# Kernel optimization log

Measured on AMD Instinct MI355X. Metric: run time of the kernel, lower is better.

Reference implementation:

```python
import jax, jax.numpy as jnp
import numpy as np

B, S, D = 4, 2048, 1024
H, E = 8, 128  # num_head, num_dim (per-head)

def setup_inputs() -> dict:
    key = jax.random.key(0)
    ks = jax.random.split(key, 8)
    scale_in = 1.0 / np.sqrt(D)
    return {
        "q": jax.random.normal(ks[0], (B, S, D), dtype=jnp.float32),
        "k": jax.random.normal(ks[1], (B, S, D), dtype=jnp.float32),
        "v": jax.random.normal(ks[2], (B, S, D), dtype=jnp.float32),
        "Wq": jax.random.normal(ks[3], (H, D, E), dtype=jnp.float32) * scale_in,
        "Wk": jax.random.normal(ks[4], (H, D, E), dtype=jnp.float32) * scale_in,
        "Wv": jax.random.normal(ks[5], (H, D, E), dtype=jnp.float32) * scale_in,
        "Wo": jax.random.normal(ks[6], (H * E, D), dtype=jnp.float32) * (1.0 / np.sqrt(H * E)),
        "bo": jnp.zeros((D,), dtype=jnp.float32),
    }

def reference(q, k, v, Wq, Wk, Wv, Wo, bo):
    dk = jnp.asarray(E, q.dtype) ** 0.5
    # per-head projections, all heads batched: [B,H,S,E]
    qh = jnp.einsum("bsd,hde->bhse", q, Wq)
    kh = jnp.einsum("bsd,hde->bhse", k, Wk)
    vh = jnp.einsum("bsd,hde->bhse", v, Wv)
    scores = jnp.einsum("bhse,bhte->bhst", qh / dk, kh)  # [B,H,S,S]
    attn = jax.nn.softmax(scores, axis=-1)
    zh = jnp.einsum("bhst,bhte->bhse", attn, vh)  # [B,H,S,E]
    # concat heads along feature dim (head order preserved): [B,S,H*E]
    z = jnp.transpose(zh, (0, 2, 1, 3)).reshape(B, S, H * E)
    return z @ Wo + bo
```

## Files before the change

### kernel.cpp

```cpp
#include <hip/hip_runtime.h>

#define B_ 4
#define S_ 2048
#define D_ 1024
#define H_ 8
#define E_ 128

typedef __bf16 bf16_t;
typedef __bf16 bf16x8 __attribute__((ext_vector_type(8)));
typedef float f32x4 __attribute__((ext_vector_type(4)));

#define MFMA16(a, b, c) __builtin_amdgcn_mfma_f32_16x16x32_bf16(a, b, c, 0, 0, 0)

#define LDP_ 72

__device__ __forceinline__ void load_lds16(const bf16_t* g, bf16_t* l) {
    __builtin_amdgcn_global_load_lds(
        (const __attribute__((address_space(1))) unsigned int*)g,
        (__attribute__((address_space(3))) unsigned int*)l,
        16, 0, 0);
}

__device__ __forceinline__ f32x4 zero4() {
    f32x4 z = {0.f, 0.f, 0.f, 0.f};
    return z;
}

__global__ __launch_bounds__(64) void detect_dtype(const unsigned int* __restrict__ q,
                                                   int* __restrict__ flag) {
    int lane = threadIdx.x;
    int cnt = 0;
    for (int i = lane; i < 4096; i += 64) {
        unsigned e = (q[i] >> 7) & 0xFFu;
        cnt += (e >= 110u && e <= 141u) ? 1 : 0;
    }
#pragma unroll
    for (int d = 32; d; d >>= 1) cnt += __shfl_down(cnt, d);
    if (lane == 0) *flag = (cnt > 2048) ? 1 : 0;
}

__global__ __launch_bounds__(256) void convert_bf16(const void* __restrict__ p0,
                                                    const void* __restrict__ p1,
                                                    const void* __restrict__ p2,
                                                    bf16_t* __restrict__ out,
                                                    const int* __restrict__ flagp) {
    const size_t QSZ = (size_t)B_ * H_ * S_ * E_;
    int z = blockIdx.z;
    const void* in = (z == 0) ? p0 : (z == 1) ? p1 : p2;
    bf16_t* o = out + (size_t)z * QSZ;
    int isb = *flagp;
    size_t i = ((size_t)blockIdx.x * 256 + threadIdx.x) * 8;
    if (isb) {
        *(bf16x8*)(o + i) = *(const bf16x8*)((const bf16_t*)in + i);
    } else {
        const float* p = (const float*)in + i;
        f32x4 lo = *(const f32x4*)p;
        f32x4 hi = *(const f32x4*)(p + 4);
        bf16x8 v;
#pragma unroll
        for (int j = 0; j < 4; j++) { v[j] = (bf16_t)lo[j]; v[4 + j] = (bf16_t)hi[j]; }
        *(bf16x8*)(o + i) = v;
    }
}

__global__ __launch_bounds__(256) void transpose_any(const void* __restrict__ p0,
                                                     const void* __restrict__ p1,
                                                     const void* __restrict__ p2,
                                                     bf16_t* __restrict__ out,
                                                     int R, int C,
                                                     const int* __restrict__ flagp) {
    __shared__ bf16_t tile[32][33];
    int isb = *flagp;
    int bz = blockIdx.z;
    int sel = bz >> 3, sub = bz & 7;
    const void* in = (sel == 0) ? p0 : (sel == 1) ? p1 : p2;
    const bf16_t* inb16 = (const bf16_t*)in + (size_t)sub * R * C;
    const float*  inb32 = (const float*)in + (size_t)sub * R * C;
    bf16_t* outb = out + (size_t)bz * R * C;
    int tx = threadIdx.x & 31, ty = threadIdx.x >> 5;
    int r0 = blockIdx.y * 32, c0 = blockIdx.x * 32;
#pragma unroll
    for (int i = 0; i < 4; i++) {
        size_t idx = (size_t)(r0 + ty + i * 8) * C + c0 + tx;
        tile[ty + i * 8][tx] = isb ? inb16[idx] : (bf16_t)inb32[idx];
    }
    __syncthreads();
#pragma unroll
    for (int i = 0; i < 4; i++)
        outb[(size_t)(c0 + ty + i * 8) * R + r0 + tx] = tile[tx][ty + i * 8];
}

__global__ __launch_bounds__(256) void proj_gemm(const bf16_t* __restrict__ Abase,
                                                 int useZ,
                                                 const bf16_t* __restrict__ WtBase,
                                                 bf16_t* __restrict__ OutBase,
                                                 float qscale, int z0) {
    __shared__ __align__(16) bf16_t Alds[128 * 64];
    __shared__ __align__(16) bf16_t Blds[128 * 64];
    const size_t WSZ = (size_t)H_ * E_ * D_;
    const size_t QSZ = (size_t)B_ * H_ * S_ * E_;
    int z = z0 + blockIdx.z;
    const bf16_t* A = Abase + (useZ ? (size_t)z * QSZ : 0);
    const bf16_t* Bt = WtBase + (size_t)z * WSZ + (size_t)blockIdx.y * E_ * D_;
    bf16_t* Out = OutBase + (size_t)z * QSZ;
    int vmode = (z == 2);
    float oscale = (z == 0) ? qscale : 1.0f;

    int m0 = blockIdx.x * 128;
    int h = blockIdx.y;
    int t = threadIdx.x;
    int w = t >> 6, lane = t & 63;
    int quad = lane >> 4, ln = lane & 15;
    int wm = (w >> 1) * 64, wn = (w & 1) * 64;

    f32x4 acc[4][4];
#pragma unroll
    for (int i = 0; i < 4; i++)
#pragma unroll
        for (int j = 0; j < 4; j++) acc[i][j] = zero4();

    for (int k0 = 0; k0 < D_; k0 += 64) {
#pragma unroll
        for (int j = 0; j < 4; j++) {
            int base = j * 256 + w * 64;
            int G = base + lane;
            int r = G >> 3, sl = G & 7;
            int c = sl ^ (r & 7);
            load_lds16(A + (size_t)(m0 + r) * D_ + k0 + c * 8, Alds + (size_t)base * 8);
            load_lds16(Bt + (size_t)r * D_ + k0 + c * 8, Blds + (size_t)base * 8);
        }
        asm volatile("s_waitcnt vmcnt(0)" ::: "memory");
        __syncthreads();

        const bf16_t* Xsrc = vmode ? Blds : Alds;
        const bf16_t* Ysrc = vmode ? Alds : Blds;
#pragma unroll
        for (int ks = 0; ks < 2; ks++) {
            bf16x8 xf[4], yf[4];
#pragma unroll
            for (int mt = 0; mt < 4; mt++) {
                int row = wm + mt * 16 + ln;
                xf[mt] = *(const bf16x8*)(Xsrc + (size_t)row * 64 +
                                          (((ks << 2) + quad) ^ (row & 7)) * 8);
            }
#pragma unroll
            for (int nt = 0; nt < 4; nt++) {
                int row = wn + nt * 16 + ln;
                yf[nt] = *(const bf16x8*)(Ysrc + (size_t)row * 64 +
                                          (((ks << 2) + quad) ^ (row & 7)) * 8);
            }
#pragma unroll
            for (int mt = 0; mt < 4; mt++)
#pragma unroll
                for (int nt = 0; nt < 4; nt++)
                    acc[mt][nt] = MFMA16(xf[mt], yf[nt], acc[mt][nt]);
        }
        __syncthreads();
    }

#pragma unroll
    for (int mt = 0; mt < 4; mt++) {
#pragma unroll
        for (int nt = 0; nt < 4; nt++) {
#pragma unroll
            for (int r = 0; r < 4; r++) {
                int M = wm + mt * 16 + quad * 4 + r;
                int N = wn + nt * 16 + ln;
                float v = acc[mt][nt][r] * oscale;
                size_t idx;
                if (vmode == 0) {
                    int g = m0 + M;
                    int b = g >> 11, s = g & 2047;
                    idx = ((size_t)((b * H_ + h) * S_ + s)) * E_ + N;
                } else {
                    int g = m0 + N;
                    int b = g >> 11, s = g & 2047;
                    idx = ((size_t)((b * H_ + h) * E_ + M)) * S_ + s;
                }
                Out[idx] = (bf16_t)v;
            }
        }
    }
}

__global__ __launch_bounds__(256, 2) void flash_attn(const bf16_t* __restrict__ Qh,
                                                     const bf16_t* __restrict__ Kh,
                                                     const bf16_t* __restrict__ Vt,
                                                     bf16_t* __restrict__ Z) {
    __shared__ __align__(16) bf16_t Klds[64 * 128];
    __shared__ __align__(16) bf16_t Vlds[128 * 64];
    __shared__ __align__(16) bf16_t Plds[4 * 32 * LDP_];
    int bh = blockIdx.y;
    int qt = blockIdx.x;
    const bf16_t* Qbh = Qh + (size_t)bh * S_ * E_;
    const bf16_t* Kbh = Kh + (size_t)bh * S_ * E_;
    const bf16_t* Vbh = Vt + (size_t)bh * E_ * S_;
    int t = threadIdx.x, w = t >> 6, lane = t & 63;
    int quad = lane >> 4, ln = lane & 15;
    bf16_t* Pw = Plds + w * 32 * LDP_;

    bf16x8 qf[2][4];
#pragma unroll
    for (int mt = 0; mt < 2; mt++)
#pragma unroll
        for (int ks = 0; ks < 4; ks++)
            qf[mt][ks] = *(const bf16x8*)(Qbh + (size_t)(qt * 128 + w * 32 + mt * 16 + ln) * E_ +
                                          ks * 32 + quad * 8);

    f32x4 oacc[2][8];
#pragma unroll
    for (int mt = 0; mt < 2; mt++)
#pragma unroll
        for (int nt = 0; nt < 8; nt++) oacc[mt][nt] = zero4();
    float rsum[2][4];
#pragma unroll
    for (int mt = 0; mt < 2; mt++)
#pragma unroll
        for (int r = 0; r < 4; r++) rsum[mt][r] = 0.f;

    int koff[4], voff[4], ldso[4];
#pragma unroll
    for (int j = 0; j < 4; j++) {
        int base = j * 256 + w * 64;
        int G = base + lane;
        int rK = G >> 4, cK = (G & 15) ^ (rK & 15);
        int rV = G >> 3, cV = (G & 7) ^ (rV & 7);
        koff[j] = rK * E_ + cK * 8;
        voff[j] = rV * S_ + cV * 8;
        ldso[j] = G * 8;
    }

    bf16x8 gK[4], gV[4];
#pragma unroll
    for (int j = 0; j < 4; j++) {
        gK[j] = *(const bf16x8*)(Kbh + koff[j]);
        gV[j] = *(const bf16x8*)(Vbh + voff[j]);
    }

    const int NT = S_ / 64;
    for (int kt = 0; kt < NT; kt++) {
#pragma unroll
        for (int j = 0; j < 4; j++) {
            *(bf16x8*)(Klds + ldso[j]) = gK[j];
            *(bf16x8*)(Vlds + ldso[j]) = gV[j];
        }
        __syncthreads();

        int ktn = (kt + 1 < NT) ? kt + 1 : kt;
#pragma unroll
        for (int j = 0; j < 4; j++) {
            gK[j] = *(const bf16x8*)(Kbh + (size_t)ktn * 64 * E_ + koff[j]);
            gV[j] = *(const bf16x8*)(Vbh + ktn * 64 + voff[j]);
        }
        __builtin_amdgcn_sched_barrier(0);

#pragma unroll
        for (int half = 0; half < 2; half++) {
#pragma unroll
            for (int ntl = 0; ntl < 2; ntl++) {
                int nt = half * 2 + ntl;
                f32x4 sacc[2];
                sacc[0] = zero4();
                sacc[1] = zero4();
                __builtin_amdgcn_s_setprio(1);
#pragma unroll
                for (int ks = 0; ks < 4; ks++) {
                    int n = nt * 16 + ln;
                    bf16x8 kf = *(const bf16x8*)(Klds + (size_t)n * 128 +
                                                 (((ks * 4 + quad) ^ ln) & 15) * 8);
#pragma unroll
                    for (int mt = 0; mt < 2; mt++) sacc[mt] = MFMA16(qf[mt][ks], kf, sacc[mt]);
                }
                __builtin_amdgcn_s_setprio(0);
#pragma unroll
                for (int mt = 0; mt < 2; mt++) {
#pragma unroll
                    for (int r = 0; r < 4; r++) {
                        float p = exp2f(sacc[mt][r] - 18.0f);
                        rsum[mt][r] += p;
                        Pw[(size_t)(mt * 16 + quad * 4 + r) * LDP_ + nt * 16 + ln] = (bf16_t)p;
                    }
                }
            }

            asm volatile("s_waitcnt lgkmcnt(0)" ::: "memory");
            {
                int ks = half;
                bf16x8 pf[2], vf[8];
#pragma unroll
                for (int mt = 0; mt < 2; mt++)
                    pf[mt] = *(const bf16x8*)(Pw + (size_t)(mt * 16 + ln) * LDP_ +
                                              ks * 32 + quad * 8);
#pragma unroll
                for (int nt = 0; nt < 8; nt++) {
                    int n = nt * 16 + ln;
                    vf[nt] = *(const bf16x8*)(Vlds + (size_t)n * 64 +
                                              (((ks * 4 + quad) ^ n) & 7) * 8);
                }
                __builtin_amdgcn_s_setprio(1);
#pragma unroll
                for (int mt = 0; mt < 2; mt++)
#pragma unroll
                    for (int nt = 0; nt < 8; nt++)
                        oacc[mt][nt] = MFMA16(pf[mt], vf[nt], oacc[mt][nt]);
                __builtin_amdgcn_s_setprio(0);
            }
        }
        __syncthreads();
    }

    float lr[2][4];
#pragma unroll
    for (int mt = 0; mt < 2; mt++)
#pragma unroll
        for (int r = 0; r < 4; r++) {
            float v = rsum[mt][r];
#pragma unroll
            for (int d = 1; d < 16; d <<= 1) v += __shfl_xor(v, d);
            lr[mt][r] = v;
        }

    int b = bh >> 3, h = bh & 7;
#pragma unroll
    for (int mt = 0; mt < 2; mt++) {
#pragma unroll
        for (int nt = 0; nt < 8; nt++) {
#pragma unroll
            for (int r = 0; r < 4; r++) {
                int s = qt * 128 + w * 32 + mt * 16 + quad * 4 + r;
                int col = h * E_ + nt * 16 + ln;
                Z[((size_t)(b * S_ + s)) * (H_ * E_) + col] =
                    (bf16_t)(oacc[mt][nt][r] / lr[mt][r]);
            }
        }
    }
}

__global__ __launch_bounds__(256) void final_gemm(const bf16_t* __restrict__ A,
                                                  const bf16_t* __restrict__ Bt,
                                                  const void* __restrict__ bias,
                                                  void* __restrict__ Out,
                                                  const int* __restrict__ flagp) {
    __shared__ __align__(16) bf16_t Alds[128 * 64];
    __shared__ __align__(16) bf16_t Blds[128 * 64];
    int isb = *flagp;
    int m0 = blockIdx.x * 128;
    int n0 = blockIdx.y * 128;
    int t = threadIdx.x;
    int w = t >> 6, lane = t & 63;
    int quad = lane >> 4, ln = lane & 15;
    int wm = (w >> 1) * 64, wn = (w & 1) * 64;

    f32x4 acc[4][4];
#pragma unroll
    for (int i = 0; i < 4; i++)
#pragma unroll
        for (int j = 0; j < 4; j++) acc[i][j] = zero4();

    for (int k0 = 0; k0 < D_; k0 += 64) {
#pragma unroll
        for (int j = 0; j < 4; j++) {
            int base = j * 256 + w * 64;
            int G = base + lane;
            int r = G >> 3, sl = G & 7;
            int c = sl ^ (r & 7);
            load_lds16(A + (size_t)(m0 + r) * (H_ * E_) + k0 + c * 8, Alds + (size_t)base * 8);
            load_lds16(Bt + (size_t)(n0 + r) * (H_ * E_) + k0 + c * 8, Blds + (size_t)base * 8);
        }
        asm volatile("s_waitcnt vmcnt(0)" ::: "memory");
        __syncthreads();

#pragma unroll
        for (int ks = 0; ks < 2; ks++) {
            bf16x8 af[4], bfr[4];
#pragma unroll
            for (int mt = 0; mt < 4; mt++) {
                int row = wm + mt * 16 + ln;
                af[mt] = *(const bf16x8*)(Alds + (size_t)row * 64 +
                                          (((ks << 2) + quad) ^ (row & 7)) * 8);
            }
#pragma unroll
            for (int nt = 0; nt < 4; nt++) {
                int row = wn + nt * 16 + ln;
                bfr[nt] = *(const bf16x8*)(Blds + (size_t)row * 64 +
                                           (((ks << 2) + quad) ^ (row & 7)) * 8);
            }
#pragma unroll
            for (int mt = 0; mt < 4; mt++)
#pragma unroll
                for (int nt = 0; nt < 4; nt++)
                    acc[mt][nt] = MFMA16(af[mt], bfr[nt], acc[mt][nt]);
        }
        __syncthreads();
    }

#pragma unroll
    for (int mt = 0; mt < 4; mt++) {
#pragma unroll
        for (int nt = 0; nt < 4; nt++) {
#pragma unroll
            for (int r = 0; r < 4; r++) {
                int grow = m0 + wm + mt * 16 + quad * 4 + r;
                int col = n0 + wn + nt * 16 + ln;
                float bv = isb ? (float)((const bf16_t*)bias)[col]
                               : ((const float*)bias)[col];
                float v = acc[mt][nt][r] + bv;
                size_t idx = (size_t)grow * D_ + col;
                if (isb) ((bf16_t*)Out)[idx] = (bf16_t)v;
                else     ((float*)Out)[idx] = v;
            }
        }
    }
}

extern "C" void kernel_launch(void* const* d_in, const int* in_sizes, int n_in,
                              void* d_out, int out_size, void* d_ws, size_t ws_size,
                              hipStream_t stream) {
    const void* q  = d_in[0];
    const void* k  = d_in[1];
    const void* v  = d_in[2];
    const void* Wq = d_in[3];
    const void* Wk = d_in[4];
    const void* Wv = d_in[5];
    const void* Wo = d_in[6];
    const void* bo = d_in[7];

    int* flag = (int*)d_ws;
    bf16_t* arena = (bf16_t*)((char*)d_ws + 256);
    const size_t WSZ = (size_t)H_ * E_ * D_;
    const size_t QSZ = (size_t)B_ * H_ * S_ * E_;
    bf16_t* wqt = arena;
    bf16_t* wot = wqt + 3 * WSZ;

    const size_t bigBytes = 256 + 2 * (4 * WSZ + 6 * QSZ);
    const bool big = (ws_size >= bigBytes);

    dim3 blk(256);
    const float qscale = 0.08838834764831845f * 1.44269504088896340f;

    detect_dtype<<<dim3(1), dim3(64), 0, stream>>>((const unsigned int*)q, flag);
    transpose_any<<<dim3(4, 32, 24), blk, 0, stream>>>(Wq, Wk, Wv, wqt, D_, E_, flag);
    transpose_any<<<dim3(32, 32, 1), blk, 0, stream>>>(Wo, Wo, Wo, wot, H_ * E_, D_, flag);

    if (big) {
        bf16_t* conv0 = wot + WSZ;
        bf16_t* Qh = conv0 + 3 * QSZ;
        bf16_t* Kh = Qh + QSZ;
        bf16_t* Vt = Kh + QSZ;
        bf16_t* Z  = conv0;

        convert_bf16<<<dim3(4096, 1, 3), blk, 0, stream>>>(q, k, v, conv0, flag);
        proj_gemm<<<dim3(64, 8, 3), blk, 0, stream>>>(conv0, 1, wqt, Qh, qscale, 0);
        flash_attn<<<dim3(16, 32), blk, 0, stream>>>(Qh, Kh, Vt, Z);
        final_gemm<<<dim3(64, 8), blk, 0, stream>>>(Z, wot, bo, d_out, flag);
    } else {
        bf16_t* conv = wot + WSZ;
        bf16_t* Qh = conv + QSZ;
        bf16_t* Kh = Qh + QSZ;
        bf16_t* Vt = Kh + QSZ;
        bf16_t* Z  = conv;

        convert_bf16<<<dim3(4096, 1, 1), blk, 0, stream>>>(q, q, q, conv, flag);
        proj_gemm<<<dim3(64, 8, 1), blk, 0, stream>>>(conv, 0, wqt, Qh, qscale, 0);
        convert_bf16<<<dim3(4096, 1, 1), blk, 0, stream>>>(k, k, k, conv, flag);
        proj_gemm<<<dim3(64, 8, 1), blk, 0, stream>>>(conv, 0, wqt, Qh, qscale, 1);
        convert_bf16<<<dim3(4096, 1, 1), blk, 0, stream>>>(v, v, v, conv, flag);
        proj_gemm<<<dim3(64, 8, 1), blk, 0, stream>>>(conv, 0, wqt, Qh, qscale, 2);
        flash_attn<<<dim3(16, 32), blk, 0, stream>>>(Qh, Kh, Vt, Z);
        final_gemm<<<dim3(64, 8), blk, 0, stream>>>(Z, wot, bo, d_out, flag);
    }
}
```

Before: 374.5 us.

## Transpose QK^T MFMA operands to write P as packed rows and simplify row-sum

Swaps the MFMA operand order so each lane holds four consecutive key columns of one query row. P can then be stored to LDS as a packed 4-element bf16 vector instead of four scalar stores, and the row sum becomes one accumulator per lane reduced with two shuffles. The PV MFMAs now run once per tile after all four score subtiles, instead of interleaved per half, and the final normalization multiplies by a reciprocal instead of dividing. This cuts LDS store instructions and reduction work, but removes the interleaving of exp work with PV MFMAs.

```diff
diff --git a/kernel.cpp b/kernel.cpp
--- a/kernel.cpp
+++ b/kernel.cpp
@@ -7,6 +7,7 @@
 #define E_ 128
 
 typedef __bf16 bf16_t;
+typedef __bf16 bf16x4 __attribute__((ext_vector_type(4)));
 typedef __bf16 bf16x8 __attribute__((ext_vector_type(8)));
 typedef float f32x4 __attribute__((ext_vector_type(4)));
 
@@ -212,11 +213,7 @@
     for (int mt = 0; mt < 2; mt++)
 #pragma unroll
         for (int nt = 0; nt < 8; nt++) oacc[mt][nt] = zero4();
-    float rsum[2][4];
-#pragma unroll
-    for (int mt = 0; mt < 2; mt++)
-#pragma unroll
-        for (int r = 0; r < 4; r++) rsum[mt][r] = 0.f;
+    float rsum[2] = {0.f, 0.f};
 
     int koff[4], voff[4], ldso[4];
 #pragma unroll
@@ -255,70 +252,67 @@
         __builtin_amdgcn_sched_barrier(0);
 
 #pragma unroll
-        for (int half = 0; half < 2; half++) {
-#pragma unroll
-            for (int ntl = 0; ntl < 2; ntl++) {
-                int nt = half * 2 + ntl;
-                f32x4 sacc[2];
-                sacc[0] = zero4();
-                sacc[1] = zero4();
-                __builtin_amdgcn_s_setprio(1);
-#pragma unroll
-                for (int ks = 0; ks < 4; ks++) {
-                    int n = nt * 16 + ln;
-                    bf16x8 kf = *(const bf16x8*)(Klds + (size_t)n * 128 +
-                                                 (((ks * 4 + quad) ^ ln) & 15) * 8);
-#pragma unroll
-                    for (int mt = 0; mt < 2; mt++) sacc[mt] = MFMA16(qf[mt][ks], kf, sacc[mt]);
+        for (int nt = 0; nt < 4; nt++) {
+            f32x4 sacc[2];
+            sacc[0] = zero4();
+            sacc[1] = zero4();
+            __builtin_amdgcn_s_setprio(1);
+#pragma unroll
+            for (int ks = 0; ks < 4; ks++) {
+                int n = nt * 16 + ln;
+                bf16x8 kf = *(const bf16x8*)(Klds + (size_t)n * 128 +
+                                             (((ks * 4 + quad) ^ ln) & 15) * 8);
+#pragma unroll
+                for (int mt = 0; mt < 2; mt++) sacc[mt] = MFMA16(kf, qf[mt][ks], sacc[mt]);
+            }
+            __builtin_amdgcn_s_setprio(0);
+#pragma unroll
+            for (int mt = 0; mt < 2; mt++) {
+                bf16x4 pk;
+#pragma unroll
+                for (int r = 0; r < 4; r++) {
+                    float p = exp2f(sacc[mt][r] - 18.0f);
+                    rsum[mt] += p;
+                    pk[r] = (bf16_t)p;
                 }
-                __builtin_amdgcn_s_setprio(0);
-#pragma unroll
-                for (int mt = 0; mt < 2; mt++) {
-#pragma unroll
-                    for (int r = 0; r < 4; r++) {
-                        float p = exp2f(sacc[mt][r] - 18.0f);
-                        rsum[mt][r] += p;
-                        Pw[(size_t)(mt * 16 + quad * 4 + r) * LDP_ + nt * 16 + ln] = (bf16_t)p;
-                    }
-                }
-            }
-
-            asm volatile("s_waitcnt lgkmcnt(0)" ::: "memory");
-            {
-                int ks = half;
-                bf16x8 pf[2], vf[8];
-#pragma unroll
-                for (int mt = 0; mt < 2; mt++)
-                    pf[mt] = *(const bf16x8*)(Pw + (size_t)(mt * 16 + ln) * LDP_ +
-                                              ks * 32 + quad * 8);
-#pragma unroll
-                for (int nt = 0; nt < 8; nt++) {
-                    int n = nt * 16 + ln;
-                    vf[nt] = *(const bf16x8*)(Vlds + (size_t)n * 64 +
-                                              (((ks * 4 + quad) ^ n) & 7) * 8);
-                }
-                __builtin_amdgcn_s_setprio(1);
-#pragma unroll
-                for (int mt = 0; mt < 2; mt++)
-#pragma unroll
-                    for (int nt = 0; nt < 8; nt++)
-                        oacc[mt][nt] = MFMA16(pf[mt], vf[nt], oacc[mt][nt]);
-                __builtin_amdgcn_s_setprio(0);
-            }
-        }
-        __syncthreads();
-    }
-
-    float lr[2][4];
-#pragma unroll
-    for (int mt = 0; mt < 2; mt++)
-#pragma unroll
-        for (int r = 0; r < 4; r++) {
-            float v = rsum[mt][r];
-#pragma unroll
-            for (int d = 1; d < 16; d <<= 1) v += __shfl_xor(v, d);
-            lr[mt][r] = v;
-        }
+                *(bf16x4*)(Pw + (size_t)(mt * 16 + ln) * LDP_ + nt * 16 + quad * 4) = pk;
+            }
+        }
+
+        asm volatile("s_waitcnt lgkmcnt(0)" ::: "memory");
+
+        __builtin_amdgcn_s_setprio(1);
+#pragma unroll
+        for (int ks = 0; ks < 2; ks++) {
+            bf16x8 pf[2], vf[8];
+#pragma unroll
+            for (int mt = 0; mt < 2; mt++)
+                pf[mt] = *(const bf16x8*)(Pw + (size_t)(mt * 16 + ln) * LDP_ + ks * 32 + quad * 8);
+#pragma unroll
+            for (int nt = 0; nt < 8; nt++) {
+                int n = nt * 16 + ln;
+                vf[nt] = *(const bf16x8*)(Vlds + (size_t)n * 64 +
+                                          (((ks * 4 + quad) ^ n) & 7) * 8);
+            }
+#pragma unroll
+            for (int mt = 0; mt < 2; mt++)
+#pragma unroll
+                for (int nt = 0; nt < 8; nt++)
+                    oacc[mt][nt] = MFMA16(pf[mt], vf[nt], oacc[mt][nt]);
+        }
+        __builtin_amdgcn_s_setprio(0);
+        __syncthreads();
+    }
+
+    float linv[2][4];
+#pragma unroll
+    for (int mt = 0; mt < 2; mt++) {
+        float v = rsum[mt];
+        v += __shfl_xor(v, 16);
+        v += __shfl_xor(v, 32);
+#pragma unroll
+        for (int r = 0; r < 4; r++) linv[mt][r] = 1.0f / __shfl(v, quad * 4 + r);
+    }
 
     int b = bh >> 3, h = bh & 7;
 #pragma unroll
@@ -330,7 +324,7 @@
                 int s = qt * 128 + w * 32 + mt * 16 + quad * 4 + r;
                 int col = h * E_ + nt * 16 + ln;
                 Z[((size_t)(b * S_ + s)) * (H_ * E_) + col] =
-                    (bf16_t)(oacc[mt][nt][r] / lr[mt][r]);
+                    (bf16_t)(oacc[mt][nt][r] * linv[mt][r]);
             }
         }
     }
```

Measured after the change: 377.8 us. Within noise of the previous version (+0.9%).
